# Kernel optimization log

Measured on AMD Instinct MI355X. Metric: run time of the kernel, lower is better.

## Reference

```python
import jax, jax.numpy as jnp
import numpy as np

B, IN, D1, H1, H2, NC = 16384, 1024, 8, 2048, 1024, 1000
C = IN // D1  # 128 channels, D=8 each
EPS = 1e-5


def _bn(x, g, b):
    # training-mode BatchNorm1d: biased variance over batch dim
    m = jnp.mean(x, axis=0)
    v = jnp.var(x, axis=0)
    return (x - m) * jax.lax.rsqrt(v + EPS) * g + b


def setup_inputs() -> dict:
    key = jax.random.key(0)
    ks = jax.random.split(key, 18)
    f = jax.random.normal
    return {
        "x": f(ks[0], (B, IN), jnp.float32),
        "norm0_g": 1.0 + 0.1 * f(ks[1], (IN,), jnp.float32),
        "norm0_b": 0.1 * f(ks[2], (IN,), jnp.float32),
        "S": f(ks[3], (C, D1, 15), jnp.float32),
        "Hm": f(ks[4], (15, 16), jnp.float32),
        "T": f(ks[5], (C, 15), jnp.float32),
        "LUT": f(ks[6], (C, 16, D1), jnp.float32),
        "W1": 0.02 * f(ks[7], (H1, IN), jnp.float32),
        "b1": 0.02 * f(ks[8], (H1,), jnp.float32),
        "norm1_g": 1.0 + 0.1 * f(ks[9], (H1,), jnp.float32),
        "norm1_b": 0.1 * f(ks[10], (H1,), jnp.float32),
        "W2": 0.02 * f(ks[11], (H2, H1), jnp.float32),
        "b2": 0.02 * f(ks[12], (H2,), jnp.float32),
        "norm2_g": 1.0 + 0.1 * f(ks[13], (H2,), jnp.float32),
        "norm2_b": 0.1 * f(ks[14], (H2,), jnp.float32),
        "W3": 0.02 * f(ks[15], (NC, H2), jnp.float32),
        "b3": 0.02 * f(ks[16], (NC,), jnp.float32),
    }


def reference(x, norm0_g, norm0_b, S, Hm, T, LUT, W1, b1,
              norm1_g, norm1_b, W2, b2, norm2_g, norm2_b, W3, b3):
    h = _bn(x, norm0_g, norm0_b)
    # --- MM block: per-channel small GEMMs + STE sign + STE argmax LUT ---
    xc = h.reshape(-1, C, D1)                          # [B, C, D]
    z = jnp.einsum('bcd,cdk->bck', xc, S) - T - 1e-4   # [B, C, 15]
    t = jnp.tanh(z)
    q = jax.lax.stop_gradient(jnp.sign(z) - t) + t     # STE sign
    logits = jnp.einsum('bck,kj->bcj', q, Hm)          # [B, C, 16]
    one_hot = jax.nn.one_hot(jnp.argmax(logits, axis=-1), 16, dtype=logits.dtype)
    sm = jax.nn.softmax(logits, axis=-1)
    oh_out = jnp.einsum('bck,ckd->bcd', one_hot, LUT)
    sm_out = jnp.einsum('bck,ckd->bcd', sm, LUT)
    v = jax.lax.stop_gradient(oh_out - sm_out) + sm_out  # STE argmax select
    v = v.reshape(-1, C * D1)                           # [B, IN]
    # --- MLP head ---
    h1 = jax.nn.relu(_bn(v @ W1.T + b1, norm1_g, norm1_b))
    h2 = jax.nn.relu(_bn(h1 @ W2.T + b2, norm2_g, norm2_b))
    logits3 = h2 @ W3.T + b3
    return jax.nn.log_softmax(logits3, axis=-1), h1
```

## Files before the change

### kernel.cpp

```cpp
#include <hip/hip_runtime.h>

typedef unsigned short u16;
typedef __attribute__((ext_vector_type(8))) short bf16x8;
typedef __attribute__((ext_vector_type(4))) float f32x4;
typedef __attribute__((ext_vector_type(4))) u16 u16x4;
typedef __attribute__((ext_vector_type(8))) u16 u16x8;

__device__ __forceinline__ u16 f2bf(float f) {
    union { float f; unsigned u; } v; v.f = f;
    unsigned u = v.u;
    unsigned r = (u + 0x7fffu + ((u >> 16) & 1u)) >> 16;
    return (u16)r;
}
__device__ __forceinline__ float bf2f(u16 u) {
    union { unsigned u; float f; } v; v.u = ((unsigned)u) << 16;
    return v.f;
}

__device__ __forceinline__ void gload16(const u16* g, u16* l) {
    __builtin_amdgcn_global_load_lds((const __attribute__((address_space(1))) void*)g,
                                     (__attribute__((address_space(3))) void*)l, 16, 0, 0);
}

#define WAITV(N) asm volatile("s_waitcnt vmcnt(" #N ")" ::: "memory")

__device__ __forceinline__ void sbar() {
    __builtin_amdgcn_sched_barrier(0);
    __builtin_amdgcn_s_barrier();
    __builtin_amdgcn_sched_barrier(0);
}

__device__ __forceinline__ void cvt4(const float* in, u16* out, int i) {
    f32x4 v = *(const f32x4*)(in + (size_t)i * 4);
    u16x4 o;
    o.x = f2bf(v.x); o.y = f2bf(v.y); o.z = f2bf(v.z); o.w = f2bf(v.w);
    *(u16x4*)(out + (size_t)i * 4) = o;
}

__global__ __launch_bounds__(256) void cvt_all_kernel(
    const float* __restrict__ W1, const float* __restrict__ W2, const float* __restrict__ W3,
    u16* __restrict__ W1b, u16* __restrict__ W2b, u16* __restrict__ W3b) {
    int i = blockIdx.x * 256 + threadIdx.x;
    if (i < 524288) {
        cvt4(W1, W1b, i);
    } else if (i < 1048576) {
        cvt4(W2, W2b, i - 524288);
    } else {
        int j = i - 1048576;
        int e = j * 4;
        int row = e >> 10;
        u16x4 o;
        if (row < 1000) {
            f32x4 v = *(const f32x4*)(W3 + e);
            o.x = f2bf(v.x); o.y = f2bf(v.y); o.z = f2bf(v.z); o.w = f2bf(v.w);
        } else {
            o.x = 0; o.y = 0; o.z = 0; o.w = 0;
        }
        *(u16x4*)(W3b + e) = o;
    }
}

template <typename DT>
__global__ __launch_bounds__(256) void col_stats_partial(
    const DT* __restrict__ X, int cols, int rows_per, float* __restrict__ part) {
    int col = (blockIdx.x * 256 + threadIdx.x) * 4;
    long base = (long)blockIdx.y * rows_per * cols + col;
    f32x4 s = {0.f, 0.f, 0.f, 0.f};
    f32x4 q = {0.f, 0.f, 0.f, 0.f};
    for (int r = 0; r < rows_per; ++r) {
        f32x4 v = *(const f32x4*)(X + base + (long)r * cols);
        s.x += v.x; s.y += v.y; s.z += v.z; s.w += v.w;
        q.x = fmaf(v.x, v.x, q.x); q.y = fmaf(v.y, v.y, q.y);
        q.z = fmaf(v.z, v.z, q.z); q.w = fmaf(v.w, v.w, q.w);
    }
    long o = ((long)blockIdx.y * cols + col) * 2;
    f32x4 p0 = {s.x, q.x, s.y, q.y};
    f32x4 p1 = {s.z, q.z, s.w, q.w};
    *(f32x4*)(part + o) = p0;
    *(f32x4*)(part + o + 4) = p1;
}

__global__ __launch_bounds__(256) void col_stats_finalize(
    const float* __restrict__ part, int cols, int nblk, float inv_n,
    const float* __restrict__ g, const float* __restrict__ b, float* __restrict__ ab) {
    __shared__ float red[8][64];
    int cl = threadIdx.x & 31;
    int j = threadIdx.x >> 5;
    int col = blockIdx.x * 32 + cl;
    int per = nblk / 8;
    float s = 0.f, ss = 0.f;
    for (int i = 0; i < per; ++i) {
        long o = ((long)(j * per + i) * cols + col) * 2;
        s += part[o]; ss += part[o + 1];
    }
    red[j][cl * 2] = s;
    red[j][cl * 2 + 1] = ss;
    __syncthreads();
    if (threadIdx.x < 32) {
        int c = blockIdx.x * 32 + threadIdx.x;
        float fs = 0.f, fss = 0.f;
#pragma unroll
        for (int jj = 0; jj < 8; ++jj) {
            fs += red[jj][threadIdx.x * 2];
            fss += red[jj][threadIdx.x * 2 + 1];
        }
        float m = fs * inv_n;
        float var = fss * inv_n - m * m;
        float a = g[c] * rsqrtf(var + 1e-5f);
        ab[c * 2 + 0] = a;
        ab[c * 2 + 1] = b[c] - m * a;
    }
}

__global__ __launch_bounds__(256) void mm_block_kernel(
    const float* __restrict__ x, const float* __restrict__ ab0,
    const float* __restrict__ S, const float* __restrict__ Tt,
    const float* __restrict__ Hm, const float* __restrict__ LUT,
    u16* __restrict__ v) {
    __shared__ float sS[480];
    __shared__ float sT[60];
    __shared__ float sHm[240];
    __shared__ float sLUT[512];
    __shared__ float sAB[64];
    const int t = threadIdx.x;
    const int cb = blockIdx.y * 4;

    for (int i = t; i < 480; i += 256) sS[i] = S[cb * 120 + i];
    for (int i = t; i < 60; i += 256)  sT[i] = Tt[cb * 15 + i];
    for (int i = t; i < 240; i += 256) sHm[i] = Hm[i];
    for (int i = t; i < 512; i += 256) sLUT[i] = LUT[cb * 128 + i];
    for (int i = t; i < 64; i += 256)  sAB[i] = ab0[cb * 16 + i];
    __syncthreads();

    const int row = blockIdx.x * 256 + t;
    const float* xp = x + (size_t)row * 1024 + cb * 8;
    float xr[32];
#pragma unroll
    for (int i = 0; i < 8; ++i) {
        f32x4 v4 = *(const f32x4*)(xp + i * 4);
        xr[i * 4 + 0] = v4.x; xr[i * 4 + 1] = v4.y;
        xr[i * 4 + 2] = v4.z; xr[i * 4 + 3] = v4.w;
    }
    u16 ov[32];
#pragma unroll
    for (int ch = 0; ch < 4; ++ch) {
        float h[8];
#pragma unroll
        for (int d = 0; d < 8; ++d)
            h[d] = xr[ch * 8 + d] * sAB[ch * 16 + d * 2] + sAB[ch * 16 + d * 2 + 1];
        float lg[16];
#pragma unroll
        for (int j = 0; j < 16; ++j) lg[j] = 0.f;
        for (int k = 0; k < 15; ++k) {
            float a = 0.f;
#pragma unroll
            for (int d = 0; d < 8; ++d) a = fmaf(h[d], sS[ch * 120 + d * 15 + k], a);
            float z = (a - sT[ch * 15 + k]) - 1e-4f;
            float q = (z > 0.f) ? 1.f : ((z < 0.f) ? -1.f : 0.f);
#pragma unroll
            for (int j = 0; j < 16; ++j) lg[j] = fmaf(q, sHm[k * 16 + j], lg[j]);
        }
        int jb = 0; float best = lg[0];
#pragma unroll
        for (int j = 1; j < 16; ++j) { if (lg[j] > best) { best = lg[j]; jb = j; } }
#pragma unroll
        for (int d = 0; d < 8; ++d) ov[ch * 8 + d] = f2bf(sLUT[ch * 128 + jb * 8 + d]);
    }
    u16* vp = v + (size_t)row * 1024 + cb * 8;
#pragma unroll
    for (int ch = 0; ch < 4; ++ch)
        *(u16x8*)(vp + ch * 8) = *(u16x8*)&ov[ch * 8];
}

__global__ __launch_bounds__(256) void bn_relu_apply8(
    const u16* __restrict__ y, const float* __restrict__ ab, int cols, int total8,
    float* __restrict__ out_f32, u16* __restrict__ out_b16) {
    int i = blockIdx.x * 256 + threadIdx.x;
    if (i >= total8) return;
    long e = (long)i * 8;
    int col = (int)(e % cols);
    u16x8 yv = *(const u16x8*)(y + e);
    float r[8];
#pragma unroll
    for (int d = 0; d < 8; ++d)
        r[d] = fmaxf(bf2f(yv[d]) * ab[(col + d) * 2] + ab[(col + d) * 2 + 1], 0.f);
    if (out_f32) {
        f32x4 rf0 = {r[0], r[1], r[2], r[3]};
        f32x4 rf1 = {r[4], r[5], r[6], r[7]};
        *(f32x4*)(out_f32 + e) = rf0;
        *(f32x4*)(out_f32 + e + 4) = rf1;
    }
    u16x8 o;
#pragma unroll
    for (int d = 0; d < 8; ++d) o[d] = f2bf(r[d]);
    *(u16x8*)(out_b16 + e) = o;
}

#define MFMA16(a, b, c) __builtin_amdgcn_mfma_f32_16x16x32_bf16(a, b, c, 0, 0, 0)

template <bool STORE_BF16, bool DO_STATS>
__global__ __launch_bounds__(512, 2) void gemm256(
    const u16* __restrict__ A, const u16* __restrict__ Bm, void* __restrict__ Cv,
    const float* __restrict__ bias, float* __restrict__ part,
    int M, int N, int K, int ldc, int ncol) {
    extern __shared__ u16 lds[];
    const int BOFF = 32768;
    const int t = threadIdx.x, lane = t & 63, w = t >> 6;
    const int wr = w >> 2, wc = w & 3;
    const int fr = lane & 15, kg = lane >> 4;
    const int gx = gridDim.x, nwg = gx * gridDim.y;
    const int flat = blockIdx.y * gx + blockIdx.x;
    const int swz = (flat & 7) * (nwg >> 3) + (flat >> 3);
    const int bm = (swz % gx) * 256;
    const int bn = (swz / gx) * 256;
    const int NT = K >> 6;

    const int srow8 = lane >> 3;
    const int scc = (lane & 7) ^ srow8;
    const int L0 = w * 2;
    const u16* gAb = A + ((size_t)bm + L0 * 8 + srow8) * K + scc * 8;
    const u16* gBb = Bm + ((size_t)bn + L0 * 8 + srow8) * K + scc * 8;
    u16* ldsW = lds + L0 * 512 + lane * 8;

    const int s0 = (kg ^ (fr & 7)) * 8;
    const int s1 = s0 ^ 32;
    int rA[4], rB[2];
#pragma unroll
    for (int i = 0; i < 4; ++i) rA[i] = (i * 32 + wr * 16 + fr) * 64;
#pragma unroll
    for (int p = 0; p < 2; ++p) rB[p] = (p * 64 + wc * 16 + fr) * 64;

    f32x4 acc[8][4];
#pragma unroll
    for (int m = 0; m < 8; ++m)
#pragma unroll
        for (int n = 0; n < 4; ++n) acc[m][n] = (f32x4){0.f, 0.f, 0.f, 0.f};

    bf16x8 Ar[8][2], Br[2][2];

#define STG(gp, matOff, d, half, k0)                                          \
    {                                                                         \
        u16* dst_ = ldsW + (matOff) + ((d) * 2 + (half)) * 8192;              \
        const u16* src_ = (gp) + (size_t)((half) * 128) * K + (k0);           \
        gload16(src_, dst_);                                                  \
        gload16(src_ + (size_t)8 * K, dst_ + 512);                            \
    }
#define LDF(off) (*(const bf16x8*)&lds[off])

    STG(gAb, 0, 0, 0, 0);
    STG(gBb, BOFF, 0, 0, 0);
    STG(gAb, 0, 0, 1, 0);
    STG(gBb, BOFF, 0, 1, 0);

#pragma unroll 2
    for (int tt = 0; tt < NT - 1; ++tt) {
        const int d = tt & 1, dn = d ^ 1;
        const int k0n = (tt + 1) << 6;
        const int a0 = (d * 2) * 8192, a1 = (d * 2 + 1) * 8192;
        const int b0 = BOFF + a0, b1 = BOFF + a1;
        WAITV(4); sbar();
        STG(gAb, 0, dn, 0, k0n);
#pragma unroll
        for (int i = 0; i < 4; ++i) { Ar[i][0] = LDF(a0 + rA[i] + s0); Ar[i][1] = LDF(a0 + rA[i] + s1); }
#pragma unroll
        for (int p = 0; p < 2; ++p) { Br[p][0] = LDF(b0 + rB[p] + s0); Br[p][1] = LDF(b0 + rB[p] + s1); }
        __builtin_amdgcn_s_setprio(1);
#pragma unroll
        for (int i = 0; i < 4; ++i)
#pragma unroll
            for (int p = 0; p < 2; ++p) {
                acc[i][p] = MFMA16(Ar[i][0], Br[p][0], acc[i][p]);
                acc[i][p] = MFMA16(Ar[i][1], Br[p][1], acc[i][p]);
            }
        __builtin_amdgcn_s_setprio(0);
        WAITV(4); sbar();
        STG(gBb, BOFF, dn, 0, k0n);
#pragma unroll
        for (int i = 0; i < 4; ++i) { Ar[4 + i][0] = LDF(a1 + rA[i] + s0); Ar[4 + i][1] = LDF(a1 + rA[i] + s1); }
        __builtin_amdgcn_s_setprio(1);
#pragma unroll
        for (int i = 0; i < 4; ++i)
#pragma unroll
            for (int p = 0; p < 2; ++p) {
                acc[4 + i][p] = MFMA16(Ar[4 + i][0], Br[p][0], acc[4 + i][p]);
                acc[4 + i][p] = MFMA16(Ar[4 + i][1], Br[p][1], acc[4 + i][p]);
            }
        __builtin_amdgcn_s_setprio(0);
        WAITV(4); sbar();
        STG(gAb, 0, dn, 1, k0n);
#pragma unroll
        for (int p = 0; p < 2; ++p) { Br[p][0] = LDF(b1 + rB[p] + s0); Br[p][1] = LDF(b1 + rB[p] + s1); }
        __builtin_amdgcn_s_setprio(1);
#pragma unroll
        for (int i = 0; i < 4; ++i)
#pragma unroll
            for (int p = 0; p < 2; ++p) {
                acc[4 + i][2 + p] = MFMA16(Ar[4 + i][0], Br[p][0], acc[4 + i][2 + p]);
                acc[4 + i][2 + p] = MFMA16(Ar[4 + i][1], Br[p][1], acc[4 + i][2 + p]);
            }
        __builtin_amdgcn_s_setprio(0);
        STG(gBb, BOFF, dn, 1, k0n);
        __builtin_amdgcn_s_setprio(1);
#pragma unroll
        for (int i = 0; i < 4; ++i)
#pragma unroll
            for (int p = 0; p < 2; ++p) {
                acc[i][2 + p] = MFMA16(Ar[i][0], Br[p][0], acc[i][2 + p]);
                acc[i][2 + p] = MFMA16(Ar[i][1], Br[p][1], acc[i][2 + p]);
            }
        __builtin_amdgcn_s_setprio(0);
    }
    {
        const int d = (NT - 1) & 1;
        const int a0 = (d * 2) * 8192, a1 = (d * 2 + 1) * 8192;
        const int b0 = BOFF + a0, b1 = BOFF + a1;
        WAITV(4); sbar();
#pragma unroll
        for (int i = 0; i < 4; ++i) { Ar[i][0] = LDF(a0 + rA[i] + s0); Ar[i][1] = LDF(a0 + rA[i] + s1); }
#pragma unroll
        for (int p = 0; p < 2; ++p) { Br[p][0] = LDF(b0 + rB[p] + s0); Br[p][1] = LDF(b0 + rB[p] + s1); }
        __builtin_amdgcn_s_setprio(1);
#pragma unroll
        for (int i = 0; i < 4; ++i)
#pragma unroll
            for (int p = 0; p < 2; ++p) {
                acc[i][p] = MFMA16(Ar[i][0], Br[p][0], acc[i][p]);
                acc[i][p] = MFMA16(Ar[i][1], Br[p][1], acc[i][p]);
            }
        __builtin_amdgcn_s_setprio(0);
        WAITV(2); sbar();
#pragma unroll
        for (int i = 0; i < 4; ++i) { Ar[4 + i][0] = LDF(a1 + rA[i] + s0); Ar[4 + i][1] = LDF(a1 + rA[i] + s1); }
        __builtin_amdgcn_s_setprio(1);
#pragma unroll
        for (int i = 0; i < 4; ++i)
#pragma unroll
            for (int p = 0; p < 2; ++p) {
                acc[4 + i][p] = MFMA16(Ar[4 + i][0], Br[p][0], acc[4 + i][p]);
                acc[4 + i][p] = MFMA16(Ar[4 + i][1], Br[p][1], acc[4 + i][p]);
            }
        __builtin_amdgcn_s_setprio(0);
        WAITV(0); sbar();
#pragma unroll
        for (int p = 0; p < 2; ++p) { Br[p][0] = LDF(b1 + rB[p] + s0); Br[p][1] = LDF(b1 + rB[p] + s1); }
        __builtin_amdgcn_s_setprio(1);
#pragma unroll
        for (int i = 0; i < 4; ++i)
#pragma unroll
            for (int p = 0; p < 2; ++p) {
                acc[4 + i][2 + p] = MFMA16(Ar[4 + i][0], Br[p][0], acc[4 + i][2 + p]);
                acc[4 + i][2 + p] = MFMA16(Ar[4 + i][1], Br[p][1], acc[4 + i][2 + p]);
                acc[i][2 + p] = MFMA16(Ar[i][0], Br[p][0], acc[i][2 + p]);
                acc[i][2 + p] = MFMA16(Ar[i][1], Br[p][1], acc[i][2 + p]);
            }
        __builtin_amdgcn_s_setprio(0);
    }

    const int fq = lane >> 4;
#pragma unroll
    for (int m = 0; m < 8; ++m) {
#pragma unroll
        for (int n = 0; n < 4; ++n) {
            int row = bm + m * 32 + wr * 16 + fq * 4;
            int col = bn + n * 64 + wc * 16 + fr;
            if (STORE_BF16) {
                u16* C = (u16*)Cv;
#pragma unroll
                for (int j = 0; j < 4; ++j)
                    C[(size_t)(row + j) * ldc + col] = f2bf(acc[m][n][j]);
            } else {
                if (col < ncol) {
                    float* C = (float*)Cv;
                    float bv = bias ? bias[col] : 0.f;
#pragma unroll
                    for (int j = 0; j < 4; ++j)
                        C[(size_t)(row + j) * ldc + col] = acc[m][n][j] + bv;
                }
            }
        }
    }

    if (DO_STATS) {
        __syncthreads();
        float* smf = (float*)lds;
        float sv[4], qv[4];
#pragma unroll
        for (int n = 0; n < 4; ++n) {
            float s = 0.f, q = 0.f;
#pragma unroll
            for (int m = 0; m < 8; ++m)
#pragma unroll
                for (int j = 0; j < 4; ++j) {
                    float vv = acc[m][n][j];
                    s += vv;
                    q = fmaf(vv, vv, q);
                }
            s += __shfl_xor(s, 16); s += __shfl_xor(s, 32);
            q += __shfl_xor(q, 16); q += __shfl_xor(q, 32);
            sv[n] = s; qv[n] = q;
        }
        if (lane < 16) {
#pragma unroll
            for (int n = 0; n < 4; ++n) {
                smf[(w * 64 + n * 16 + lane) * 2 + 0] = sv[n];
                smf[(w * 64 + n * 16 + lane) * 2 + 1] = qv[n];
            }
        }
        __syncthreads();
        if (t < 256) {
            int n = t >> 6, wcq = (t >> 4) & 3, frq = t & 15;
            int i0 = (wcq * 64 + n * 16 + frq) * 2;
            int i1 = ((4 + wcq) * 64 + n * 16 + frq) * 2;
            long o = ((long)(bm >> 8) * N + bn + t) * 2;
            part[o] = smf[i0] + smf[i1];
            part[o + 1] = smf[i0 + 1] + smf[i1 + 1];
        }
    }
#undef STG
#undef LDF
}

__global__ __launch_bounds__(256) void log_softmax_wave(float* __restrict__ y) {
    const int w = threadIdx.x >> 6;
    const int lane = threadIdx.x & 63;
    float* p = y + ((size_t)blockIdx.x * 4 + w) * 1000;
    float m = -1e30f;
    for (int c = lane; c < 250; c += 64) {
        f32x4 v = ((const f32x4*)p)[c];
        m = fmaxf(m, fmaxf(fmaxf(v.x, v.y), fmaxf(v.z, v.w)));
    }
#pragma unroll
    for (int d = 32; d > 0; d >>= 1) m = fmaxf(m, __shfl_xor(m, d));
    float sum = 0.f;
    for (int c = lane; c < 250; c += 64) {
        f32x4 v = ((const f32x4*)p)[c];
        sum += expf(v.x - m) + expf(v.y - m) + expf(v.z - m) + expf(v.w - m);
    }
#pragma unroll
    for (int d = 32; d > 0; d >>= 1) sum += __shfl_xor(sum, d);
    float lse = m + logf(sum);
    for (int c = lane; c < 250; c += 64) {
        f32x4 v = ((const f32x4*)p)[c];
        v.x -= lse; v.y -= lse; v.z -= lse; v.w -= lse;
        ((f32x4*)p)[c] = v;
    }
}

extern "C" void kernel_launch(void* const* d_in, const int* in_sizes, int n_in,
                              void* d_out, int out_size, void* d_ws, size_t ws_size,
                              hipStream_t stream) {
    const float* x   = (const float*)d_in[0];
    const float* n0g = (const float*)d_in[1];
    const float* n0b = (const float*)d_in[2];
    const float* S   = (const float*)d_in[3];
    const float* Hm  = (const float*)d_in[4];
    const float* Tt  = (const float*)d_in[5];
    const float* LUT = (const float*)d_in[6];
    const float* W1  = (const float*)d_in[7];
    const float* n1g = (const float*)d_in[9];
    const float* n1b = (const float*)d_in[10];
    const float* W2  = (const float*)d_in[11];
    const float* n2g = (const float*)d_in[13];
    const float* n2b = (const float*)d_in[14];
    const float* W3  = (const float*)d_in[15];
    const float* b3  = (const float*)d_in[16];

    const int B = 16384, IN = 1024, H1 = 2048, H2 = 1024;
    const int NBY0 = 512;

    hipFuncSetAttribute((const void*)&gemm256<true, true>,
                        hipFuncAttributeMaxDynamicSharedMemorySize, 131072);
    hipFuncSetAttribute((const void*)&gemm256<false, false>,
                        hipFuncAttributeMaxDynamicSharedMemorySize, 131072);

    char* ws = (char*)d_ws;
    size_t off = 0;
    auto alloc = [&](size_t bytes) -> char* {
        char* p = ws + off;
        off += (bytes + 255) & ~(size_t)255;
        return p;
    };
    float* ab0  = (float*)alloc(IN * 2 * sizeof(float));
    float* ab1  = (float*)alloc(H1 * 2 * sizeof(float));
    float* ab2  = (float*)alloc(H2 * 2 * sizeof(float));
    float* part0 = (float*)alloc((size_t)NBY0 * IN * 2 * sizeof(float));
    float* part1 = (float*)alloc((size_t)(B / 256) * H1 * 2 * sizeof(float));
    float* part2 = (float*)alloc((size_t)(B / 256) * H2 * 2 * sizeof(float));
    u16* W1b = (u16*)alloc((size_t)H1 * IN * 2);
    u16* W2b = (u16*)alloc((size_t)H2 * H1 * 2);
    u16* W3b = (u16*)alloc((size_t)1024 * 1024 * 2);
    u16* vb  = (u16*)alloc((size_t)B * IN * 2);
    u16* y1b = (u16*)alloc((size_t)B * H1 * 2);

    float* out0 = (float*)d_out;
    float* out1 = out0 + (size_t)B * 1000;

    cvt_all_kernel<<<5120, 256, 0, stream>>>(W1, W2, W3, W1b, W2b, W3b);

    col_stats_partial<float><<<dim3(1, NBY0), 256, 0, stream>>>(x, IN, B / NBY0, part0);
    col_stats_finalize<<<IN / 32, 256, 0, stream>>>(part0, IN, NBY0, 1.f / B, n0g, n0b, ab0);

    mm_block_kernel<<<dim3(B / 256, 32), 256, 0, stream>>>(x, ab0, S, Tt, Hm, LUT, vb);

    gemm256<true, true><<<dim3(B / 256, H1 / 256), 512, 131072, stream>>>(
        vb, W1b, y1b, nullptr, part1, B, H1, IN, H1, H1);
    col_stats_finalize<<<H1 / 32, 256, 0, stream>>>(part1, H1, B / 256, 1.f / B, n1g, n1b, ab1);
    bn_relu_apply8<<<B * H1 / 8 / 256, 256, 0, stream>>>(y1b, ab1, H1, B * H1 / 8, out1, y1b);

    gemm256<true, true><<<dim3(B / 256, H2 / 256), 512, 131072, stream>>>(
        y1b, W2b, vb, nullptr, part2, B, H2, H1, H2, H2);
    col_stats_finalize<<<H2 / 32, 256, 0, stream>>>(part2, H2, B / 256, 1.f / B, n2g, n2b, ab2);
    bn_relu_apply8<<<B * H2 / 8 / 256, 256, 0, stream>>>(vb, ab2, H2, B * H2 / 8, nullptr, vb);

    gemm256<false, false><<<dim3(B / 256, 1024 / 256), 512, 131072, stream>>>(
        vb, W3b, out0, b3, nullptr, B, 1024, H2, 1000, 1000);

    log_softmax_wave<<<B / 4, 256, 0, stream>>>(out0);
}
```

Baseline: 370.0 us.

## Fuse weight conversion with BN0 stats, stage bf16 GEMM stores via LDS, register log-softmax

Merges the weight bf16 conversion and the input column-stats partial pass into one launch, which saves a kernel launch and lets the two independent jobs overlap. The bf16 GEMM epilogue now stages each 32-row slab in LDS and writes 16-byte coalesced vectors instead of scattered 2-byte stores, at the cost of extra barriers. The log-softmax keeps each row in registers, so it reads global memory once instead of three times. The stats branch hardcodes 32 rows per block, so it is only correct when NBY0 equals 512.

```diff
diff --git a/kernel.cpp b/kernel.cpp
--- a/kernel.cpp
+++ b/kernel.cpp
@@ -37,47 +37,48 @@
     *(u16x4*)(out + (size_t)i * 4) = o;
 }
 
-__global__ __launch_bounds__(256) void cvt_all_kernel(
+__global__ __launch_bounds__(256) void leaf_kernel(
     const float* __restrict__ W1, const float* __restrict__ W2, const float* __restrict__ W3,
-    u16* __restrict__ W1b, u16* __restrict__ W2b, u16* __restrict__ W3b) {
-    int i = blockIdx.x * 256 + threadIdx.x;
-    if (i < 524288) {
-        cvt4(W1, W1b, i);
-    } else if (i < 1048576) {
-        cvt4(W2, W2b, i - 524288);
+    u16* __restrict__ W1b, u16* __restrict__ W2b, u16* __restrict__ W3b,
+    const float* __restrict__ x, float* __restrict__ part0) {
+    int bid = blockIdx.x;
+    if (bid < 5120) {
+        int i = bid * 256 + threadIdx.x;
+        if (i < 524288) {
+            cvt4(W1, W1b, i);
+        } else if (i < 1048576) {
+            cvt4(W2, W2b, i - 524288);
+        } else {
+            int j = i - 1048576;
+            int e = j * 4;
+            int row = e >> 10;
+            u16x4 o;
+            if (row < 1000) {
+                f32x4 v = *(const f32x4*)(W3 + e);
+                o.x = f2bf(v.x); o.y = f2bf(v.y); o.z = f2bf(v.z); o.w = f2bf(v.w);
+            } else {
+                o.x = 0; o.y = 0; o.z = 0; o.w = 0;
+            }
+            *(u16x4*)(W3b + e) = o;
+        }
     } else {
-        int j = i - 1048576;
-        int e = j * 4;
-        int row = e >> 10;
-        u16x4 o;
-        if (row < 1000) {
-            f32x4 v = *(const f32x4*)(W3 + e);
-            o.x = f2bf(v.x); o.y = f2bf(v.y); o.z = f2bf(v.z); o.w = f2bf(v.w);
-        } else {
-            o.x = 0; o.y = 0; o.z = 0; o.w = 0;
-        }
-        *(u16x4*)(W3b + e) = o;
-    }
-}
-
-template <typename DT>
-__global__ __launch_bounds__(256) void col_stats_partial(
-    const DT* __restrict__ X, int cols, int rows_per, float* __restrict__ part) {
-    int col = (blockIdx.x * 256 + threadIdx.x) * 4;
-    long base = (long)blockIdx.y * rows_per * cols + col;
-    f32x4 s = {0.f, 0.f, 0.f, 0.f};
-    f32x4 q = {0.f, 0.f, 0.f, 0.f};
-    for (int r = 0; r < rows_per; ++r) {
-        f32x4 v = *(const f32x4*)(X + base + (long)r * cols);
-        s.x += v.x; s.y += v.y; s.z += v.z; s.w += v.w;
-        q.x = fmaf(v.x, v.x, q.x); q.y = fmaf(v.y, v.y, q.y);
-        q.z = fmaf(v.z, v.z, q.z); q.w = fmaf(v.w, v.w, q.w);
-    }
-    long o = ((long)blockIdx.y * cols + col) * 2;
-    f32x4 p0 = {s.x, q.x, s.y, q.y};
-    f32x4 p1 = {s.z, q.z, s.w, q.w};
-    *(f32x4*)(part + o) = p0;
-    *(f32x4*)(part + o + 4) = p1;
+        int by = bid - 5120;
+        int col = threadIdx.x * 4;
+        long base = (long)by * 32 * 1024 + col;
+        f32x4 s = {0.f, 0.f, 0.f, 0.f};
+        f32x4 q = {0.f, 0.f, 0.f, 0.f};
+        for (int r = 0; r < 32; ++r) {
+            f32x4 v = *(const f32x4*)(x + base + (long)r * 1024);
+            s.x += v.x; s.y += v.y; s.z += v.z; s.w += v.w;
+            q.x = fmaf(v.x, v.x, q.x); q.y = fmaf(v.y, v.y, q.y);
+            q.z = fmaf(v.z, v.z, q.z); q.w = fmaf(v.w, v.w, q.w);
+        }
+        long o = ((long)by * 1024 + col) * 2;
+        f32x4 p0 = {s.x, q.x, s.y, q.y};
+        f32x4 p1 = {s.z, q.z, s.w, q.w};
+        *(f32x4*)(part0 + o) = p0;
+        *(f32x4*)(part0 + o + 4) = p1;
+    }
 }
 
 __global__ __launch_bounds__(256) void col_stats_finalize(
@@ -357,18 +358,33 @@
     }
 
     const int fq = lane >> 4;
-#pragma unroll
-    for (int m = 0; m < 8; ++m) {
-#pragma unroll
-        for (int n = 0; n < 4; ++n) {
-            int row = bm + m * 32 + wr * 16 + fq * 4;
-            int col = bn + n * 64 + wc * 16 + fr;
-            if (STORE_BF16) {
-                u16* C = (u16*)Cv;
+    if (STORE_BF16) {
+        u16* C = (u16*)Cv;
+        u16* sm = lds;
+        const int orow = t >> 4;
+        const int ocol = (t & 15) * 16;
+#pragma unroll
+        for (int m = 0; m < 8; ++m) {
+            __syncthreads();
+#pragma unroll
+            for (int n = 0; n < 4; ++n)
 #pragma unroll
                 for (int j = 0; j < 4; ++j)
-                    C[(size_t)(row + j) * ldc + col] = f2bf(acc[m][n][j]);
-            } else {
+                    sm[(wr * 16 + fq * 4 + j) * 256 + n * 64 + wc * 16 + fr] = f2bf(acc[m][n][j]);
+            __syncthreads();
+            u16x8 o0 = *(const u16x8*)&sm[orow * 256 + ocol];
+            u16x8 o1 = *(const u16x8*)&sm[orow * 256 + ocol + 8];
+            u16* cp = C + (size_t)(bm + m * 32 + orow) * ldc + bn + ocol;
+            *(u16x8*)cp = o0;
+            *(u16x8*)(cp + 8) = o1;
+        }
+    } else {
+#pragma unroll
+        for (int m = 0; m < 8; ++m) {
+#pragma unroll
+            for (int n = 0; n < 4; ++n) {
+                int row = bm + m * 32 + wr * 16 + fq * 4;
+                int col = bn + n * 64 + wc * 16 + fr;
                 if (col < ncol) {
                     float* C = (float*)Cv;
                     float bv = bias ? bias[col] : 0.f;
@@ -424,25 +440,34 @@
     const int w = threadIdx.x >> 6;
     const int lane = threadIdx.x & 63;
     float* p = y + ((size_t)blockIdx.x * 4 + w) * 1000;
-    float m = -1e30f;
-    for (int c = lane; c < 250; c += 64) {
-        f32x4 v = ((const f32x4*)p)[c];
-        m = fmaxf(m, fmaxf(fmaxf(v.x, v.y), fmaxf(v.z, v.w)));
-    }
+    const bool has3 = lane < 58;
+    f32x4 v0 = ((const f32x4*)p)[lane];
+    f32x4 v1 = ((const f32x4*)p)[lane + 64];
+    f32x4 v2 = ((const f32x4*)p)[lane + 128];
+    f32x4 v3 = has3 ? ((const f32x4*)p)[lane + 192]
+                    : (f32x4){-1e30f, -1e30f, -1e30f, -1e30f};
+    float m = fmaxf(fmaxf(fmaxf(v0.x, v0.y), fmaxf(v0.z, v0.w)),
+                    fmaxf(fmaxf(v1.x, v1.y), fmaxf(v1.z, v1.w)));
+    m = fmaxf(m, fmaxf(fmaxf(v2.x, v2.y), fmaxf(v2.z, v2.w)));
+    m = fmaxf(m, fmaxf(fmaxf(v3.x, v3.y), fmaxf(v3.z, v3.w)));
 #pragma unroll
     for (int d = 32; d > 0; d >>= 1) m = fmaxf(m, __shfl_xor(m, d));
-    float sum = 0.f;
-    for (int c = lane; c < 250; c += 64) {
-        f32x4 v = ((const f32x4*)p)[c];
-        sum += expf(v.x - m) + expf(v.y - m) + expf(v.z - m) + expf(v.w - m);
-    }
+    float sum = expf(v0.x - m) + expf(v0.y - m) + expf(v0.z - m) + expf(v0.w - m)
+              + expf(v1.x - m) + expf(v1.y - m) + expf(v1.z - m) + expf(v1.w - m)
+              + expf(v2.x - m) + expf(v2.y - m) + expf(v2.z - m) + expf(v2.w - m)
+              + expf(v3.x - m) + expf(v3.y - m) + expf(v3.z - m) + expf(v3.w - m);
 #pragma unroll
     for (int d = 32; d > 0; d >>= 1) sum += __shfl_xor(sum, d);
     float lse = m + logf(sum);
-    for (int c = lane; c < 250; c += 64) {
-        f32x4 v = ((const f32x4*)p)[c];
-        v.x -= lse; v.y -= lse; v.z -= lse; v.w -= lse;
-        ((f32x4*)p)[c] = v;
+    v0.x -= lse; v0.y -= lse; v0.z -= lse; v0.w -= lse;
+    v1.x -= lse; v1.y -= lse; v1.z -= lse; v1.w -= lse;
+    v2.x -= lse; v2.y -= lse; v2.z -= lse; v2.w -= lse;
+    ((f32x4*)p)[lane] = v0;
+    ((f32x4*)p)[lane + 64] = v1;
+    ((f32x4*)p)[lane + 128] = v2;
+    if (has3) {
+        v3.x -= lse; v3.y -= lse; v3.z -= lse; v3.w -= lse;
+        ((f32x4*)p)[lane + 192] = v3;
     }
 }
 
@@ -495,20 +520,21 @@
     float* out0 = (float*)d_out;
     float* out1 = out0 + (size_t)B * 1000;
 
-    cvt_all_kernel<<<5120, 256, 0, stream>>>(W1, W2, W3, W1b, W2b, W3b);
-
-    col_stats_partial<float><<<dim3(1, NBY0), 256, 0, stream>>>(x, IN, B / NBY0, part0);
+    leaf_kernel<<<5120 + NBY0, 256, 0, stream>>>(W1, W2, W3, W1b, W2b, W3b, x, part0);
+
     col_stats_finalize<<<IN / 32, 256, 0, stream>>>(part0, IN, NBY0, 1.f / B, n0g, n0b, ab0);
 
     mm_block_kernel<<<dim3(B / 256, 32), 256, 0, stream>>>(x, ab0, S, Tt, Hm, LUT, vb);
 
     gemm256<true, true><<<dim3(B / 256, H1 / 256), 512, 131072, stream>>>(
         vb, W1b, y1b, nullptr, part1, B, H1, IN, H1, H1);
+
     col_stats_finalize<<<H1 / 32, 256, 0, stream>>>(part1, H1, B / 256, 1.f / B, n1g, n1b, ab1);
     bn_relu_apply8<<<B * H1 / 8 / 256, 256, 0, stream>>>(y1b, ab1, H1, B * H1 / 8, out1, y1b);
 
     gemm256<true, true><<<dim3(B / 256, H2 / 256), 512, 131072, stream>>>(
         y1b, W2b, vb, nullptr, part2, B, H2, H1, H2, H2);
+
     col_stats_finalize<<<H2 / 32, 256, 0, stream>>>(part2, H2, B / 256, 1.f / B, n2g, n2b, ab2);
     bn_relu_apply8<<<B * H2 / 8 / 256, 256, 0, stream>>>(vb, ab2, H2, B * H2 / 8, nullptr, vb);
 
```

Measured after the change: 360.5 us. -2.6%, faster.
